# Kernel tuning notes

Measured on AMD Instinct MI355X. Metric: run time of the kernel, lower is better.

Reference implementation:

```python
import jax, jax.numpy as jnp
import numpy as np
import math

NUM_HEADS = 16
EMBED_DIM = 1024
DIM_HEAD = EMBED_DIM // NUM_HEADS


def setup_inputs() -> dict:
    key = jax.random.key(0)
    k_x, k_wi, k_bi, k_wo, k_bo = jax.random.split(key, 5)
    B, S, D = 2, 2048, EMBED_DIM
    scale = 1.0 / math.sqrt(D)
    return {
        "x": jax.random.normal(k_x, (B, S, D), dtype=jnp.float32),
        "w_in": jax.random.normal(k_wi, (3 * D, D), dtype=jnp.float32) * scale,
        "b_in": jax.random.normal(k_bi, (3 * D,), dtype=jnp.float32) * 0.02,
        "w_out": jax.random.normal(k_wo, (D, D), dtype=jnp.float32) * scale,
        "b_out": jax.random.normal(k_bo, (D,), dtype=jnp.float32) * 0.02,
    }


def reference(x, w_in, b_in, w_out, b_out):
    B, S, D = x.shape
    H, Dh = NUM_HEADS, DIM_HEAD
    # in_proj: x @ w_in.T + b_in -> chunk into q, k, v
    qkv = jnp.einsum("bsd,ed->bse", x, w_in) + b_in  # [B,S,3D]
    q, k, v = jnp.split(qkv, 3, axis=-1)
    q = q.reshape(B, S, H, Dh).transpose(0, 2, 1, 3)  # [B,H,S,Dh]
    k = k.reshape(B, S, H, Dh).transpose(0, 2, 1, 3)
    v = v.reshape(B, S, H, Dh).transpose(0, 2, 1, 3)
    # scores, causal mask (masked_fill before scaling == after, since -inf/c = -inf)
    scores = jnp.einsum("bhqd,bhkd->bhqk", q, k) / math.sqrt(Dh)
    causal = jnp.triu(jnp.ones((S, S), dtype=bool), k=1)
    scores = jnp.where(causal, -jnp.inf, scores)
    weight = jax.nn.softmax(scores, axis=-1)
    out = jnp.einsum("bhqk,bhkd->bhqd", weight, v)  # [B,H,S,Dh]
    out = out.transpose(0, 2, 1, 3).reshape(B, S, D)
    return jnp.einsum("bsd,ed->bse", out, w_out) + b_out
```

## Files before the change

kernel.cpp:

```cpp
#include <hip/hip_runtime.h>
#include <stdint.h>

typedef unsigned short u16;
typedef float f32x4 __attribute__((ext_vector_type(4)));
typedef __bf16 bf16x8 __attribute__((ext_vector_type(8)));

#define AS1 __attribute__((address_space(1)))
#define AS3 __attribute__((address_space(3)))

#define QK_SCALE 0.18033688011112042f

__device__ __forceinline__ u16 f32_to_bf16(float f) {
    unsigned u = __float_as_uint(f);
    unsigned r = u + 0x7fffu + ((u >> 16) & 1u);
    return (u16)(r >> 16);
}

__device__ __forceinline__ float bf16_f(u16 u) {
    return __uint_as_float(((unsigned)u) << 16);
}

__device__ __forceinline__ void gload_lds16(const u16* g, u16* l) {
    __builtin_amdgcn_global_load_lds((const AS1 unsigned int*)g,
                                     (AS3 unsigned int*)l, 16, 0, 0);
}

__device__ __forceinline__ int swz(int row, int col8) {
    return row * 64 + (((col8 ^ (row & 7)) & 7) << 3);
}
__device__ __forceinline__ int swzv(int row, int col8) {
    return row * 64 + (((col8 ^ row ^ (row >> 3)) & 7) << 3);
}

__global__ __launch_bounds__(256) void cvt_bf16_3(const float4* __restrict__ in0,
                                                  const float4* __restrict__ in1,
                                                  const float4* __restrict__ in2,
                                                  uint2* __restrict__ out,
                                                  int n0, int n1, int ntot) {
    for (int i = blockIdx.x * blockDim.x + threadIdx.x; i < ntot;
         i += gridDim.x * blockDim.x) {
        float4 v;
        if (i < n0) v = in0[i];
        else if (i < n0 + n1) {
            v = in1[i - n0];
            if (((i - n0) >> 8) < 1024) {
                v.x *= QK_SCALE; v.y *= QK_SCALE; v.z *= QK_SCALE; v.w *= QK_SCALE;
            }
        } else v = in2[i - n0 - n1];
        uint2 o;
        o.x = (unsigned)f32_to_bf16(v.x) | ((unsigned)f32_to_bf16(v.y) << 16);
        o.y = (unsigned)f32_to_bf16(v.z) | ((unsigned)f32_to_bf16(v.w) << 16);
        out[i] = o;
    }
}

template <int BNT, bool BF16_OUT>
__global__ __launch_bounds__(512, 2) void gemm_ring(const u16* __restrict__ A,
                                                    const u16* __restrict__ B,
                                                    const float* __restrict__ bias,
                                                    void* __restrict__ Cv,
                                                    int M, int N, int K,
                                                    int qcols, float qscale) {
    extern __shared__ u16 lds[];
    constexpr int NACC = BNT / 64;
    constexpr int NCH = (128 + BNT) >> 7;
    constexpr int ASZ = 128 * 32;
    constexpr int BSZ = BNT * 32;
    const int t = threadIdx.x;
    const int l = t & 63, w = t >> 6;
    const int lr = l & 15, lhi = l >> 4;
    const int wm = w >> 2, wn = w & 3;
    const int orig = blockIdx.y * gridDim.x + blockIdx.x;
    const int sid = (orig & 7) * 32 + (orig >> 3);
    const int bm = sid & 31, bn = sid >> 5;

    const u16* Ag = A + (size_t)bm * 128 * K;
    const u16* Bg = B + (size_t)bn * BNT * K;

    auto STAGE = [&](int kt, int slot) {
        u16* As = lds + slot * ASZ;
        u16* Bs = lds + 4 * ASZ + slot * BSZ;
        {
            int c = t, row = c >> 2, cp = c & 3;
            int gc = (cp ^ ((row >> 1) & 3)) << 3;
            gload_lds16(Ag + (size_t)row * K + kt * 32 + gc, As + c * 8);
        }
        #pragma unroll
        for (int i = 0; i < NCH - 1; ++i) {
            int c = i * 512 + t, row = c >> 2, cp = c & 3;
            int gc = (cp ^ ((row >> 1) & 3)) << 3;
            gload_lds16(Bg + (size_t)row * K + kt * 32 + gc, Bs + c * 8);
        }
    };

    f32x4 acc[4][NACC] = {};
    const int NT = K >> 5;
    STAGE(0, 0);
    STAGE(1, 1);
    STAGE(2, 2);

    const int ckey = (lr >> 1) & 3;

    for (int kt = 0; kt < NT; ++kt) {
        if (kt < NT - 2) {
            if constexpr (NCH == 4) asm volatile("s_waitcnt vmcnt(8)" ::: "memory");
            else                    asm volatile("s_waitcnt vmcnt(4)" ::: "memory");
        } else if (kt == NT - 2) {
            if constexpr (NCH == 4) asm volatile("s_waitcnt vmcnt(4)" ::: "memory");
            else                    asm volatile("s_waitcnt vmcnt(2)" ::: "memory");
        } else {
            asm volatile("s_waitcnt vmcnt(0)" ::: "memory");
        }
        __builtin_amdgcn_s_barrier();

        if (kt + 3 < NT) STAGE(kt + 3, (kt + 3) & 3);

        const u16* As = lds + (kt & 3) * ASZ;
        const u16* Bs = lds + 4 * ASZ + (kt & 3) * BSZ;
        bf16x8 af[4], bfv[NACC];
        #pragma unroll
        for (int m = 0; m < 4; ++m) {
            int row = wm * 64 + m * 16 + lr;
            af[m] = *(const bf16x8*)(As + row * 32 + ((lhi ^ ckey) << 3));
        }
        #pragma unroll
        for (int n = 0; n < NACC; ++n) {
            int row = wn * (BNT / 4) + n * 16 + lr;
            bfv[n] = *(const bf16x8*)(Bs + row * 32 + ((lhi ^ ckey) << 3));
        }
        asm volatile("s_waitcnt lgkmcnt(0)" ::: "memory");
        __builtin_amdgcn_sched_barrier(0);
        __builtin_amdgcn_s_setprio(1);
        #pragma unroll
        for (int m = 0; m < 4; ++m)
            #pragma unroll
            for (int n = 0; n < NACC; ++n)
                acc[m][n] = __builtin_amdgcn_mfma_f32_16x16x32_bf16(
                    af[m], bfv[n], acc[m][n], 0, 0, 0);
        __builtin_amdgcn_s_setprio(0);
    }

    const int row0 = bm * 128 + wm * 64 + lhi * 4;
    const int col0 = bn * BNT + wn * (BNT / 4) + lr;
    #pragma unroll
    for (int n = 0; n < NACC; ++n) {
        int col = col0 + n * 16;
        float bv = bias[col];
        if (col < qcols) bv *= qscale;
        #pragma unroll
        for (int m = 0; m < 4; ++m)
            #pragma unroll
            for (int r = 0; r < 4; ++r) {
                int row = row0 + m * 16 + r;
                float v = acc[m][n][r] + bv;
                if constexpr (BF16_OUT)
                    ((u16*)Cv)[(size_t)row * N + col] = f32_to_bf16(v);
                else
                    ((float*)Cv)[(size_t)row * N + col] = v;
            }
    }
}

__device__ __forceinline__ void write_vt(u16* vt, uint4 a, uint4 b, int g, int cl) {
    unsigned aw[4] = {a.x, a.y, a.z, a.w};
    unsigned bw[4] = {b.x, b.y, b.z, b.w};
    #pragma unroll
    for (int j = 0; j < 8; ++j) {
        int dh = cl * 8 + j;
        unsigned sel = (j & 1) ? 0x07060302u : 0x05040100u;
        unsigned v = __builtin_amdgcn_perm(bw[j >> 1], aw[j >> 1], sel);
        *(unsigned*)(vt + swzv(dh, g >> 2) + (2 * g & 7)) = v;
    }
}

__global__ __launch_bounds__(512, 4) void attn_kernel(const u16* __restrict__ qkv,
                                                      u16* __restrict__ out) {
    extern __shared__ u16 alds[];
    const int t = threadIdx.x;
    const int w = t >> 6, l = t & 63;
    const int lr = l & 15, lhi = l >> 4;
    const int par = w >> 2, wl = w & 3;
    const int tp = t & 255;
    const int orig = blockIdx.x;
    const int sid = (orig & 7) * 64 + (orig >> 3);
    const int bh = sid >> 4, bi = sid & 15;
    const int h = bh & 15, b = bh >> 4;

    const u16* Kg = qkv + ((size_t)(b * 2048)) * 3072 + 1024 + h * 64;
    const u16* Vg = qkv + ((size_t)(b * 2048)) * 3072 + 2048 + h * 64;
    const int vg = tp >> 3, vcl = tp & 7;
    u16* KsP = alds + par * 8192;
    u16* VtP = alds + 16384 + par * 8192;
    u16* Pw = alds + 32768 + w * 1024;
    unsigned* Pst = (unsigned*)Pw;
    float2* mlX = (float2*)alds;

    #pragma unroll 1
    for (int pass = 0; pass < 2; ++pass) {
        const int qt = pass ? (31 - bi) : bi;
        __syncthreads();

        const u16* Qrow = qkv + ((size_t)(b * 2048 + qt * 64 + wl * 16 + lr)) * 3072 + h * 64;
        bf16x8 qf0 = *(const bf16x8*)(Qrow + lhi * 8);
        bf16x8 qf1 = *(const bf16x8*)(Qrow + 32 + lhi * 8);

        #pragma unroll
        for (int i = 0; i < 2; ++i) {
            int c = i * 256 + tp, r = c >> 3, cl = c & 7;
            gload_lds16(Kg + ((size_t)(par * 64 + r)) * 3072 + ((cl ^ (r & 7)) << 3),
                        KsP + c * 8);
        }
        uint4 va0 = *(const uint4*)(Vg + ((size_t)(par * 64 + 2 * vg)) * 3072 + vcl * 8);
        uint4 vb0 = *(const uint4*)(Vg + ((size_t)(par * 64 + 2 * vg + 1)) * 3072 + vcl * 8);
        uint4 vaC = *(const uint4*)(Vg + ((size_t)((par + 2) * 64 + 2 * vg)) * 3072 + vcl * 8);
        uint4 vbC = *(const uint4*)(Vg + ((size_t)((par + 2) * 64 + 2 * vg + 1)) * 3072 + vcl * 8);
        write_vt(VtP, va0, vb0, vg, vcl);
        __syncthreads();

        f32x4 acc[4] = {};
        float m_run = -1e30f, l_run = 0.f;
        int cur = 0;
        const int nt = (qt >> 1) + 1;

        for (int it = 0; it < nt; ++it) {
            const int t64 = 2 * it + par;
            const bool active = (t64 <= qt);

            #pragma unroll
            for (int i = 0; i < 2; ++i) {
                int c = i * 256 + tp, r = c >> 3, cl = c & 7;
                gload_lds16(Kg + ((size_t)((t64 + 2) * 64 + r)) * 3072 +
                                ((cl ^ (r & 7)) << 3),
                            KsP + (cur ^ 1) * 4096 + c * 8);
            }
            uint4 vaN = *(const uint4*)(Vg + ((size_t)((t64 + 4) * 64 + 2 * vg)) * 3072 + vcl * 8);
            uint4 vbN = *(const uint4*)(Vg + ((size_t)((t64 + 4) * 64 + 2 * vg + 1)) * 3072 + vcl * 8);

            if (active) {
                const u16* Kc = KsP + cur * 4096;
                __builtin_amdgcn_s_setprio(1);
                f32x4 sv[4] = {};
                #pragma unroll
                for (int kks = 0; kks < 2; ++kks) {
                    #pragma unroll
                    for (int n = 0; n < 4; ++n) {
                        bf16x8 kf = *(const bf16x8*)(Kc + swz(n * 16 + lr, kks * 4 + lhi));
                        sv[n] = __builtin_amdgcn_mfma_f32_16x16x32_bf16(
                            kf, kks ? qf1 : qf0, sv[n], 0, 0, 0);
                    }
                }
                __builtin_amdgcn_s_setprio(0);

                if (t64 == qt) {
                    #pragma unroll
                    for (int n = 0; n < 4; ++n)
                        #pragma unroll
                        for (int r = 0; r < 4; ++r)
                            if ((n * 16 + lhi * 4 + r) > (wl * 16 + lr)) sv[n][r] = -1e30f;
                }
                float t0 = fmaxf(fmaxf(sv[0][0], sv[0][1]), fmaxf(sv[0][2], sv[0][3]));
                float t1 = fmaxf(fmaxf(sv[1][0], sv[1][1]), fmaxf(sv[1][2], sv[1][3]));
                float t2 = fmaxf(fmaxf(sv[2][0], sv[2][1]), fmaxf(sv[2][2], sv[2][3]));
                float t3 = fmaxf(fmaxf(sv[3][0], sv[3][1]), fmaxf(sv[3][2], sv[3][3]));
                float mx = fmaxf(fmaxf(t0, t1), fmaxf(t2, t3));
                mx = fmaxf(mx, __shfl_xor(mx, 16, 64));
                mx = fmaxf(mx, __shfl_xor(mx, 32, 64));

                if (__any(mx > m_run + 8.f)) {
                    float mn = fmaxf(m_run, mx);
                    float alpha = exp2f(m_run - mn);
                    m_run = mn;
                    l_run *= alpha;
                    #pragma unroll
                    for (int r = 0; r < 4; ++r) {
                        float ar = __shfl(alpha, lhi * 4 + r, 16);
                        #pragma unroll
                        for (int n = 0; n < 4; ++n) acc[n][r] *= ar;
                    }
                }

                float rs = 0.f;
                #pragma unroll
                for (int n = 0; n < 4; ++n)
                    #pragma unroll
                    for (int r = 0; r < 4; ++r) {
                        float pe = exp2f(sv[n][r] - m_run);
                        sv[n][r] = pe;
                        rs += pe;
                    }
                l_run += rs;

                #pragma unroll
                for (int n = 0; n < 4; ++n)
                    #pragma unroll
                    for (int rp = 0; rp < 2; ++rp) {
                        union { unsigned u; __bf16 hh[2]; } pk;
                        pk.hh[0] = (__bf16)sv[n][2 * rp];
                        pk.hh[1] = (__bf16)sv[n][2 * rp + 1];
                        int pp = 8 * n + 2 * lhi + rp;
                        Pst[lr * 32 + (((pp >> 2) ^ (lr & 7)) << 2) + (pp & 3)] = pk.u;
                    }
            }

            write_vt(VtP + (cur ^ 1) * 4096, vaC, vbC, vg, vcl);
            vaC = vaN; vbC = vbN;

            if (active) {
                const u16* Vc = VtP + cur * 4096;
                __builtin_amdgcn_s_setprio(1);
                #pragma unroll
                for (int kks = 0; kks < 2; ++kks) {
                    bf16x8 pa = *(const bf16x8*)(Pw + lr * 64 +
                                                 (((kks * 4 + lhi) ^ (lr & 7)) << 3));
                    #pragma unroll
                    for (int n = 0; n < 4; ++n) {
                        bf16x8 vb = *(const bf16x8*)(Vc + swzv(n * 16 + lr, kks * 4 + lhi));
                        acc[n] = __builtin_amdgcn_mfma_f32_16x16x32_bf16(pa, vb, acc[n], 0, 0, 0);
                    }
                }
                __builtin_amdgcn_s_setprio(0);
            }

            asm volatile("s_waitcnt vmcnt(2)" ::: "memory");
            __builtin_amdgcn_s_barrier();
            cur ^= 1;
        }

        l_run += __shfl_xor(l_run, 16, 64);
        l_run += __shfl_xor(l_run, 32, 64);

        if (par == 1) {
            if (lhi == 0) mlX[wl * 16 + lr] = make_float2(m_run, l_run);
            #pragma unroll
            for (int r = 0; r < 4; ++r)
                #pragma unroll
                for (int n = 0; n < 4; ++n)
                    Pw[(lhi * 4 + r) * 64 + n * 16 + lr] = f32_to_bf16(acc[n][r]);
        }
        __syncthreads();
        if (par == 0) {
            float2 m1l1 = mlX[wl * 16 + lr];
            float m = fmaxf(m_run, m1l1.x);
            float e0 = exp2f(m_run - m), e1 = exp2f(m1l1.x - m);
            float inv = 1.0f / (l_run * e0 + m1l1.y * e1);
            float c0 = e0 * inv, c1 = e1 * inv;
            const u16* Pq = alds + 32768 + (4 + wl) * 1024;
            #pragma unroll
            for (int r = 0; r < 4; ++r) {
                float c0r = __shfl(c0, lhi * 4 + r, 16);
                float c1r = __shfl(c1, lhi * 4 + r, 16);
                int qg = qt * 64 + wl * 16 + lhi * 4 + r;
                size_t base = ((size_t)(b * 2048 + qg)) * 1024 + h * 64;
                #pragma unroll
                for (int n = 0; n < 4; ++n) {
                    float v1 = bf16_f(Pq[(lhi * 4 + r) * 64 + n * 16 + lr]);
                    out[base + n * 16 + lr] = f32_to_bf16(acc[n][r] * c0r + v1 * c1r);
                }
            }
        }
    }
}

extern "C" void kernel_launch(void* const* d_in, const int* in_sizes, int n_in,
                              void* d_out, int out_size, void* d_ws, size_t ws_size,
                              hipStream_t stream) {
    const float* x = (const float*)d_in[0];
    const float* w_in = (const float*)d_in[1];
    const float* b_in = (const float*)d_in[2];
    const float* w_out = (const float*)d_in[3];
    const float* b_out = (const float*)d_in[4];
    float* out = (float*)d_out;

    u16* xb = (u16*)d_ws;
    u16* wib = xb + (size_t)4096 * 1024;
    u16* wob = wib + (size_t)3072 * 1024;
    u16* qkvb = wob + (size_t)1024 * 1024;
    u16* attnb = qkvb + (size_t)4096 * 3072;

    const int n0 = 4096 * 1024 / 4, n1 = 3072 * 1024 / 4, n2 = 1024 * 1024 / 4;
    cvt_bf16_3<<<2048, 256, 0, stream>>>((const float4*)x, (const float4*)w_in,
                                         (const float4*)w_out, (uint2*)xb,
                                         n0, n1, n0 + n1 + n2);

    (void)hipFuncSetAttribute((const void*)gemm_ring<384, true>,
                              hipFuncAttributeMaxDynamicSharedMemorySize, 131072);
    (void)hipFuncSetAttribute((const void*)gemm_ring<128, false>,
                              hipFuncAttributeMaxDynamicSharedMemorySize, 65536);
    (void)hipFuncSetAttribute((const void*)attn_kernel,
                              hipFuncAttributeMaxDynamicSharedMemorySize, 81920);

    gemm_ring<384, true><<<dim3(32, 8), 512, 131072, stream>>>(
        xb, wib, b_in, qkvb, 4096, 3072, 1024, 1024, QK_SCALE);
    attn_kernel<<<512, 512, 81920, stream>>>(qkvb, attnb);
    gemm_ring<128, false><<<dim3(32, 8), 512, 65536, stream>>>(
        attnb, wob, b_out, out, 4096, 1024, 1024, 0, 1.0f);
}
```

Baseline: 107.4 us.

## Process both causal query tiles in one KV sweep to share K/V loads

Result: slower. 161.1 us (+50.0%).

```diff
diff --git a/kernel.cpp b/kernel.cpp
--- a/kernel.cpp
+++ b/kernel.cpp
@@ -185,6 +185,7 @@
     const int sid = (orig & 7) * 64 + (orig >> 3);
     const int bh = sid >> 4, bi = sid & 15;
     const int h = bh & 15, b = bh >> 4;
+    const int qtA = bi, qtB = 31 - bi;
 
     const u16* Kg = qkv + ((size_t)(b * 2048)) * 3072 + 1024 + h * 64;
     const u16* Vg = qkv + ((size_t)(b * 2048)) * 3072 + 2048 + h * 64;
@@ -195,140 +196,149 @@
     unsigned* Pst = (unsigned*)Pw;
     float2* mlX = (float2*)alds;
 
-    #pragma unroll 1
-    for (int pass = 0; pass < 2; ++pass) {
-        const int qt = pass ? (31 - bi) : bi;
-        __syncthreads();
-
-        const u16* Qrow = qkv + ((size_t)(b * 2048 + qt * 64 + wl * 16 + lr)) * 3072 + h * 64;
-        bf16x8 qf0 = *(const bf16x8*)(Qrow + lhi * 8);
-        bf16x8 qf1 = *(const bf16x8*)(Qrow + 32 + lhi * 8);
-
+    const u16* QrowA = qkv + ((size_t)(b * 2048 + qtA * 64 + wl * 16 + lr)) * 3072 + h * 64;
+    const u16* QrowB = qkv + ((size_t)(b * 2048 + qtB * 64 + wl * 16 + lr)) * 3072 + h * 64;
+    bf16x8 qfA0 = *(const bf16x8*)(QrowA + lhi * 8);
+    bf16x8 qfA1 = *(const bf16x8*)(QrowA + 32 + lhi * 8);
+    bf16x8 qfB0 = *(const bf16x8*)(QrowB + lhi * 8);
+    bf16x8 qfB1 = *(const bf16x8*)(QrowB + 32 + lhi * 8);
+
+    #pragma unroll
+    for (int i = 0; i < 2; ++i) {
+        int c = i * 256 + tp, r = c >> 3, cl = c & 7;
+        gload_lds16(Kg + ((size_t)(par * 64 + r)) * 3072 + ((cl ^ (r & 7)) << 3),
+                    KsP + c * 8);
+    }
+    uint4 va0 = *(const uint4*)(Vg + ((size_t)(par * 64 + 2 * vg)) * 3072 + vcl * 8);
+    uint4 vb0 = *(const uint4*)(Vg + ((size_t)(par * 64 + 2 * vg + 1)) * 3072 + vcl * 8);
+    uint4 vaC = *(const uint4*)(Vg + ((size_t)((par + 2) * 64 + 2 * vg)) * 3072 + vcl * 8);
+    uint4 vbC = *(const uint4*)(Vg + ((size_t)((par + 2) * 64 + 2 * vg + 1)) * 3072 + vcl * 8);
+    write_vt(VtP, va0, vb0, vg, vcl);
+    __syncthreads();
+
+    f32x4 accA[4] = {}, accB[4] = {};
+    float mA = -1e30f, lA = 0.f, mB = -1e30f, lB = 0.f;
+    const f32x4 z4 = {0.f, 0.f, 0.f, 0.f};
+    int cur = 0;
+    int t64 = par;
+    const int nt = (qtB >> 1) + 1;
+
+    auto FRAG = [&](const bf16x8& q0, const bf16x8& q1, int qt,
+                    f32x4* acc, float& m_run, float& l_run) {
+        const u16* Kc = KsP + cur * 4096;
+        f32x4 sv[4];
+        __builtin_amdgcn_s_setprio(1);
+        #pragma unroll
+        for (int n = 0; n < 4; ++n) {
+            bf16x8 kf = *(const bf16x8*)(Kc + swz(n * 16 + lr, lhi));
+            sv[n] = __builtin_amdgcn_mfma_f32_16x16x32_bf16(kf, q0, z4, 0, 0, 0);
+        }
+        #pragma unroll
+        for (int n = 0; n < 4; ++n) {
+            bf16x8 kf = *(const bf16x8*)(Kc + swz(n * 16 + lr, 4 + lhi));
+            sv[n] = __builtin_amdgcn_mfma_f32_16x16x32_bf16(kf, q1, sv[n], 0, 0, 0);
+        }
+        __builtin_amdgcn_s_setprio(0);
+
+        if (t64 == qt) {
+            #pragma unroll
+            for (int n = 0; n < 4; ++n)
+                #pragma unroll
+                for (int r = 0; r < 4; ++r)
+                    if ((n * 16 + lhi * 4 + r) > (wl * 16 + lr)) sv[n][r] = -1e30f;
+        }
+        float t0 = fmaxf(fmaxf(sv[0][0], sv[0][1]), fmaxf(sv[0][2], sv[0][3]));
+        float t1 = fmaxf(fmaxf(sv[1][0], sv[1][1]), fmaxf(sv[1][2], sv[1][3]));
+        float t2 = fmaxf(fmaxf(sv[2][0], sv[2][1]), fmaxf(sv[2][2], sv[2][3]));
+        float t3 = fmaxf(fmaxf(sv[3][0], sv[3][1]), fmaxf(sv[3][2], sv[3][3]));
+        float mx = fmaxf(fmaxf(t0, t1), fmaxf(t2, t3));
+        mx = fmaxf(mx, __shfl_xor(mx, 16, 64));
+        mx = fmaxf(mx, __shfl_xor(mx, 32, 64));
+
+        if (__any(mx > m_run + 8.f)) {
+            float mn = fmaxf(m_run, mx);
+            float alpha = exp2f(m_run - mn);
+            m_run = mn;
+            l_run *= alpha;
+            #pragma unroll
+            for (int r = 0; r < 4; ++r) {
+                float ar = __shfl(alpha, lhi * 4 + r, 16);
+                #pragma unroll
+                for (int n = 0; n < 4; ++n) acc[n][r] *= ar;
+            }
+        }
+
+        float rs = 0.f;
+        #pragma unroll
+        for (int n = 0; n < 4; ++n)
+            #pragma unroll
+            for (int r = 0; r < 4; ++r) {
+                float pe = exp2f(sv[n][r] - m_run);
+                sv[n][r] = pe;
+                rs += pe;
+            }
+        l_run += rs;
+
+        #pragma unroll
+        for (int n = 0; n < 4; ++n)
+            #pragma unroll
+            for (int rp = 0; rp < 2; ++rp) {
+                union { unsigned u; __bf16 hh[2]; } pk;
+                pk.hh[0] = (__bf16)sv[n][2 * rp];
+                pk.hh[1] = (__bf16)sv[n][2 * rp + 1];
+                int pp = 8 * n + 2 * lhi + rp;
+                Pst[lr * 32 + (((pp >> 2) ^ (lr & 7)) << 2) + (pp & 3)] = pk.u;
+            }
+
+        const u16* Vc = VtP + cur * 4096;
+        __builtin_amdgcn_s_setprio(1);
+        #pragma unroll
+        for (int kks = 0; kks < 2; ++kks) {
+            bf16x8 pa = *(const bf16x8*)(Pw + lr * 64 +
+                                         (((kks * 4 + lhi) ^ (lr & 7)) << 3));
+            #pragma unroll
+            for (int n = 0; n < 4; ++n) {
+                bf16x8 vb = *(const bf16x8*)(Vc + swzv(n * 16 + lr, kks * 4 + lhi));
+                acc[n] = __builtin_amdgcn_mfma_f32_16x16x32_bf16(pa, vb, acc[n], 0, 0, 0);
+            }
+        }
+        __builtin_amdgcn_s_setprio(0);
+    };
+
+    for (int it = 0; it < nt; ++it) {
         #pragma unroll
         for (int i = 0; i < 2; ++i) {
             int c = i * 256 + tp, r = c >> 3, cl = c & 7;
-            gload_lds16(Kg + ((size_t)(par * 64 + r)) * 3072 + ((cl ^ (r & 7)) << 3),
-                        KsP + c * 8);
-        }
-        uint4 va0 = *(const uint4*)(Vg + ((size_t)(par * 64 + 2 * vg)) * 3072 + vcl * 8);
-        uint4 vb0 = *(const uint4*)(Vg + ((size_t)(par * 64 + 2 * vg + 1)) * 3072 + vcl * 8);
-        uint4 vaC = *(const uint4*)(Vg + ((size_t)((par + 2) * 64 + 2 * vg)) * 3072 + vcl * 8);
-        uint4 vbC = *(const uint4*)(Vg + ((size_t)((par + 2) * 64 + 2 * vg + 1)) * 3072 + vcl * 8);
-        write_vt(VtP, va0, vb0, vg, vcl);
+            gload_lds16(Kg + ((size_t)((t64 + 2) * 64 + r)) * 3072 +
+                            ((cl ^ (r & 7)) << 3),
+                        KsP + (cur ^ 1) * 4096 + c * 8);
+        }
+        uint4 vaN = *(const uint4*)(Vg + ((size_t)((t64 + 4) * 64 + 2 * vg)) * 3072 + vcl * 8);
+        uint4 vbN = *(const uint4*)(Vg + ((size_t)((t64 + 4) * 64 + 2 * vg + 1)) * 3072 + vcl * 8);
+
+        if (t64 <= qtA) FRAG(qfA0, qfA1, qtA, accA, mA, lA);
+
+        write_vt(VtP + (cur ^ 1) * 4096, vaC, vbC, vg, vcl);
+        vaC = vaN; vbC = vbN;
+
+        if (t64 <= qtB) FRAG(qfB0, qfB1, qtB, accB, mB, lB);
+
+        asm volatile("s_waitcnt vmcnt(2)" ::: "memory");
+        __builtin_amdgcn_s_barrier();
+        cur ^= 1;
+        t64 += 2;
+    }
+
+    lA += __shfl_xor(lA, 16, 64); lA += __shfl_xor(lA, 32, 64);
+    lB += __shfl_xor(lB, 16, 64); lB += __shfl_xor(lB, 32, 64);
+
+    #pragma unroll 1
+    for (int fr = 0; fr < 2; ++fr) {
+        const int qt = fr ? qtB : qtA;
+        const f32x4* acc = fr ? accB : accA;
+        const float m_run = fr ? mB : mA;
+        const float l_run = fr ? lB : lA;
         __syncthreads();
-
-        f32x4 acc[4] = {};
-        float m_run = -1e30f, l_run = 0.f;
-        int cur = 0;
-        const int nt = (qt >> 1) + 1;
-
-        for (int it = 0; it < nt; ++it) {
-            const int t64 = 2 * it + par;
-            const bool active = (t64 <= qt);
-
-            #pragma unroll
-            for (int i = 0; i < 2; ++i) {
-                int c = i * 256 + tp, r = c >> 3, cl = c & 7;
-                gload_lds16(Kg + ((size_t)((t64 + 2) * 64 + r)) * 3072 +
-                                ((cl ^ (r & 7)) << 3),
-                            KsP + (cur ^ 1) * 4096 + c * 8);
-            }
-            uint4 vaN = *(const uint4*)(Vg + ((size_t)((t64 + 4) * 64 + 2 * vg)) * 3072 + vcl * 8);
-            uint4 vbN = *(const uint4*)(Vg + ((size_t)((t64 + 4) * 64 + 2 * vg + 1)) * 3072 + vcl * 8);
-
-            if (active) {
-                const u16* Kc = KsP + cur * 4096;
-                __builtin_amdgcn_s_setprio(1);
-                f32x4 sv[4] = {};
-                #pragma unroll
-                for (int kks = 0; kks < 2; ++kks) {
-                    #pragma unroll
-                    for (int n = 0; n < 4; ++n) {
-                        bf16x8 kf = *(const bf16x8*)(Kc + swz(n * 16 + lr, kks * 4 + lhi));
-                        sv[n] = __builtin_amdgcn_mfma_f32_16x16x32_bf16(
-                            kf, kks ? qf1 : qf0, sv[n], 0, 0, 0);
-                    }
-                }
-                __builtin_amdgcn_s_setprio(0);
-
-                if (t64 == qt) {
-                    #pragma unroll
-                    for (int n = 0; n < 4; ++n)
-                        #pragma unroll
-                        for (int r = 0; r < 4; ++r)
-                            if ((n * 16 + lhi * 4 + r) > (wl * 16 + lr)) sv[n][r] = -1e30f;
-                }
-                float t0 = fmaxf(fmaxf(sv[0][0], sv[0][1]), fmaxf(sv[0][2], sv[0][3]));
-                float t1 = fmaxf(fmaxf(sv[1][0], sv[1][1]), fmaxf(sv[1][2], sv[1][3]));
-                float t2 = fmaxf(fmaxf(sv[2][0], sv[2][1]), fmaxf(sv[2][2], sv[2][3]));
-                float t3 = fmaxf(fmaxf(sv[3][0], sv[3][1]), fmaxf(sv[3][2], sv[3][3]));
-                float mx = fmaxf(fmaxf(t0, t1), fmaxf(t2, t3));
-                mx = fmaxf(mx, __shfl_xor(mx, 16, 64));
-                mx = fmaxf(mx, __shfl_xor(mx, 32, 64));
-
-                if (__any(mx > m_run + 8.f)) {
-                    float mn = fmaxf(m_run, mx);
-                    float alpha = exp2f(m_run - mn);
-                    m_run = mn;
-                    l_run *= alpha;
-                    #pragma unroll
-                    for (int r = 0; r < 4; ++r) {
-                        float ar = __shfl(alpha, lhi * 4 + r, 16);
-                        #pragma unroll
-                        for (int n = 0; n < 4; ++n) acc[n][r] *= ar;
-                    }
-                }
-
-                float rs = 0.f;
-                #pragma unroll
-                for (int n = 0; n < 4; ++n)
-                    #pragma unroll
-                    for (int r = 0; r < 4; ++r) {
-                        float pe = exp2f(sv[n][r] - m_run);
-                        sv[n][r] = pe;
-                        rs += pe;
-                    }
-                l_run += rs;
-
-                #pragma unroll
-                for (int n = 0; n < 4; ++n)
-                    #pragma unroll
-                    for (int rp = 0; rp < 2; ++rp) {
-                        union { unsigned u; __bf16 hh[2]; } pk;
-                        pk.hh[0] = (__bf16)sv[n][2 * rp];
-                        pk.hh[1] = (__bf16)sv[n][2 * rp + 1];
-                        int pp = 8 * n + 2 * lhi + rp;
-                        Pst[lr * 32 + (((pp >> 2) ^ (lr & 7)) << 2) + (pp & 3)] = pk.u;
-                    }
-            }
-
-            write_vt(VtP + (cur ^ 1) * 4096, vaC, vbC, vg, vcl);
-            vaC = vaN; vbC = vbN;
-
-            if (active) {
-                const u16* Vc = VtP + cur * 4096;
-                __builtin_amdgcn_s_setprio(1);
-                #pragma unroll
-                for (int kks = 0; kks < 2; ++kks) {
-                    bf16x8 pa = *(const bf16x8*)(Pw + lr * 64 +
-                                                 (((kks * 4 + lhi) ^ (lr & 7)) << 3));
-                    #pragma unroll
-                    for (int n = 0; n < 4; ++n) {
-                        bf16x8 vb = *(const bf16x8*)(Vc + swzv(n * 16 + lr, kks * 4 + lhi));
-                        acc[n] = __builtin_amdgcn_mfma_f32_16x16x32_bf16(pa, vb, acc[n], 0, 0, 0);
-                    }
-                }
-                __builtin_amdgcn_s_setprio(0);
-            }
-
-            asm volatile("s_waitcnt vmcnt(2)" ::: "memory");
-            __builtin_amdgcn_s_barrier();
-            cur ^= 1;
-        }
-
-        l_run += __shfl_xor(l_run, 16, 64);
-        l_run += __shfl_xor(l_run, 32, 64);
-
         if (par == 1) {
             if (lhi == 0) mlX[wl * 16 + lr] = make_float2(m_run, l_run);
             #pragma unroll
```
